# Kernel tuning notes

Hardware: AMD Instinct MI355X
Metric: run time of the kernel (lower is better)

The kernel has to match this reference:

```python
import jax, jax.numpy as jnp
import numpy as np

ITERATION = 10

def setup_inputs() -> dict:
    key = jax.random.key(0)
    k1, k2, k3 = jax.random.split(key, 3)
    a_inter = jax.random.normal(k1, (8, 64, 64, 32, 32), dtype=jnp.float32)
    logits = jax.random.normal(k2, (8, 64), dtype=jnp.float32)
    W = jax.random.normal(k3, (1, 64, 64), dtype=jnp.float32)
    return {"a_inter": a_inter, "logits": logits, "W": W}


def reference(a_inter, logits, W):
    N = W.shape[1]  # num_nodes
    B = a_inter.shape[0]
    # feats: [B, N, C*H*W]
    feats = a_inter[:, :, :N, :, :].reshape(B, N, -1)
    # expand logits [B, N] -> [B, N, N] (unsqueeze(1).expand in torch)
    logits0 = jnp.broadcast_to(logits[:, None, :], (B, N, N))

    feats_norm = jnp.linalg.norm(feats, ord=2, axis=2, keepdims=True)  # [B, N, 1]
    pairwise_norm = feats_norm @ jnp.swapaxes(feats_norm, 1, 2)        # [B, N, N]
    pairwise_dot = feats @ jnp.swapaxes(feats, 1, 2)                   # [B, N, N]
    pairwise_sim = pairwise_dot / (pairwise_norm + 1e-6)
    W_sym = (W + jnp.swapaxes(W, 1, 2)) / 2.0
    pairwise_potential = pairwise_sim * W_sym                          # [B, N, N]

    unary_potential = logits0

    def body(i, l):
        probs = jnp.swapaxes(jax.nn.sigmoid(l), 1, 2)  # [B, N, N]
        # probs*pp - (1-probs)*pp == (2*probs - 1)*pp
        pp_E = jnp.sum((2.0 * probs - 1.0) * pairwise_potential, axis=2, keepdims=True)
        return unary_potential + pp_E

    logits_out = jax.lax.fori_loop(0, ITERATION, body, logits0)
    return logits_out.mean(axis=1)  # [B, N]
```

## Files before the change

### kernel.cpp

```cpp
#include <hip/hip_runtime.h>
#include <math.h>

#define BATCH 8
#define NN 64
#define DD 65536
#define BPB 64
#define NBLK (BATCH * BPB)
#define KC (DD / BPB)
#define KW (KC / 4)
#define KSTEPS (KW / 32)
#define NTRI 10
#define PSZ (NTRI * 256)

typedef float  floatx4 __attribute__((ext_vector_type(4)));
typedef __bf16 bf16x8  __attribute__((ext_vector_type(8)));

static __device__ __forceinline__ bf16x8 cvt8(float4 lo, float4 hi) {
    const unsigned sel = 0x07060302u;
    union { unsigned u[4]; bf16x8 v; } r;
    r.u[0] = __builtin_amdgcn_perm(__float_as_uint(lo.y), __float_as_uint(lo.x), sel);
    r.u[1] = __builtin_amdgcn_perm(__float_as_uint(lo.w), __float_as_uint(lo.z), sel);
    r.u[2] = __builtin_amdgcn_perm(__float_as_uint(hi.y), __float_as_uint(hi.x), sel);
    r.u[3] = __builtin_amdgcn_perm(__float_as_uint(hi.w), __float_as_uint(hi.z), sel);
    return r.v;
}

__global__ __launch_bounds__(256, 2) void gram_partial_kernel(const float* __restrict__ a,
                                                              float* __restrict__ part) {
    __shared__ __align__(16) float red[3][NTRI][64][4];

    const int bid = blockIdx.x;
    const int b = bid >> 6;
    const int c = bid & (BPB - 1);

    const int tid  = threadIdx.x;
    const int w    = tid >> 6;
    const int lane = tid & 63;
    const int m    = lane & 15;
    const int q    = lane >> 4;

    const float* base = a + (size_t)b * NN * DD + (size_t)c * KC + (size_t)w * KW
                          + (size_t)m * DD + q * 8;
    const float* p0 = base;
    const float* p1 = base + (size_t)16 * DD;
    const float* p2 = base + (size_t)32 * DD;
    const float* p3 = base + (size_t)48 * DD;

    floatx4 acc[NTRI];
    #pragma unroll
    for (int i = 0; i < NTRI; ++i) acc[i] = (floatx4)0.0f;

    float4 A0, A1, A2, A3, A4, A5, A6, A7;
    float4 B0, B1, B2, B3, B4, B5, B6, B7;

#define LOADSET(R0,R1,R2,R3,R4,R5,R6,R7, o)                                \
    R0 = *(const float4*)(p0 + (o));  R1 = *(const float4*)(p0 + (o) + 4); \
    R2 = *(const float4*)(p1 + (o));  R3 = *(const float4*)(p1 + (o) + 4); \
    R4 = *(const float4*)(p2 + (o));  R5 = *(const float4*)(p2 + (o) + 4); \
    R6 = *(const float4*)(p3 + (o));  R7 = *(const float4*)(p3 + (o) + 4); \
    __builtin_amdgcn_sched_barrier(0);

#define MFMASET(R0,R1,R2,R3,R4,R5,R6,R7)                                   \
    {                                                                      \
        bf16x8 f0 = cvt8(R0, R1);                                          \
        bf16x8 f1 = cvt8(R2, R3);                                          \
        bf16x8 f2 = cvt8(R4, R5);                                          \
        bf16x8 f3 = cvt8(R6, R7);                                          \
        acc[0] = __builtin_amdgcn_mfma_f32_16x16x32_bf16(f0, f0, acc[0], 0, 0, 0); \
        acc[1] = __builtin_amdgcn_mfma_f32_16x16x32_bf16(f0, f1, acc[1], 0, 0, 0); \
        acc[2] = __builtin_amdgcn_mfma_f32_16x16x32_bf16(f0, f2, acc[2], 0, 0, 0); \
        acc[3] = __builtin_amdgcn_mfma_f32_16x16x32_bf16(f0, f3, acc[3], 0, 0, 0); \
        acc[4] = __builtin_amdgcn_mfma_f32_16x16x32_bf16(f1, f1, acc[4], 0, 0, 0); \
        acc[5] = __builtin_amdgcn_mfma_f32_16x16x32_bf16(f1, f2, acc[5], 0, 0, 0); \
        acc[6] = __builtin_amdgcn_mfma_f32_16x16x32_bf16(f1, f3, acc[6], 0, 0, 0); \
        acc[7] = __builtin_amdgcn_mfma_f32_16x16x32_bf16(f2, f2, acc[7], 0, 0, 0); \
        acc[8] = __builtin_amdgcn_mfma_f32_16x16x32_bf16(f2, f3, acc[8], 0, 0, 0); \
        acc[9] = __builtin_amdgcn_mfma_f32_16x16x32_bf16(f3, f3, acc[9], 0, 0, 0); \
    }

    LOADSET(A0,A1,A2,A3,A4,A5,A6,A7, 0)
    #pragma unroll
    for (int s = 0; s < KSTEPS; s += 2) {
        LOADSET(B0,B1,B2,B3,B4,B5,B6,B7, (s + 1) * 32)
        MFMASET(A0,A1,A2,A3,A4,A5,A6,A7)
        if (s + 2 < KSTEPS) { LOADSET(A0,A1,A2,A3,A4,A5,A6,A7, (s + 2) * 32) }
        MFMASET(B0,B1,B2,B3,B4,B5,B6,B7)
    }
#undef LOADSET
#undef MFMASET

    if (w > 0) {
        #pragma unroll
        for (int t = 0; t < NTRI; ++t)
            *(floatx4*)&red[w - 1][t][lane][0] = acc[t];
    }
    __syncthreads();
    if (w == 0) {
        #pragma unroll
        for (int t = 0; t < NTRI; ++t) {
            floatx4 r0 = *(const floatx4*)&red[0][t][lane][0];
            floatx4 r1 = *(const floatx4*)&red[1][t][lane][0];
            floatx4 r2 = *(const floatx4*)&red[2][t][lane][0];
            acc[t] += (r0 + r1) + r2;
        }
        float* pg = part + (size_t)bid * PSZ;
        #pragma unroll
        for (int t = 0; t < NTRI; ++t) {
            float* tp = pg + t * 256 + m;
            #pragma unroll
            for (int r = 0; r < 4; ++r)
                tp[(q * 4 + r) * 16] = acc[t][r];
        }
    }
}

__global__ __launch_bounds__(128) void gram_reduce_kernel(const float* __restrict__ part,
                                                          float* __restrict__ gram) {
    const int gid = blockIdx.x * 128 + threadIdx.x;
    const int b   = gid >> 12;
    const int idx = gid & 4095;
    const int i   = idx >> 6;
    const int j   = idx & 63;
    const int ti  = i >> 4, tj = j >> 4;
    const int ib  = ti <= tj ? ti : tj;
    const int jb  = ti <= tj ? tj : ti;
    const int slot = ib * 4 - (ib * (ib - 1)) / 2 + (jb - ib);
    const int rr  = (ti <= tj) ? (i & 15) : (j & 15);
    const int cc  = (ti <= tj) ? (j & 15) : (i & 15);
    const int off = slot * 256 + rr * 16 + cc;
    const float* p = part + (size_t)b * BPB * PSZ + off;

    float s0 = 0.f, s1 = 0.f, s2 = 0.f, s3 = 0.f;
    #pragma unroll 4
    for (int c = 0; c < BPB; c += 4) {
        s0 += p[(size_t)(c + 0) * PSZ];
        s1 += p[(size_t)(c + 1) * PSZ];
        s2 += p[(size_t)(c + 2) * PSZ];
        s3 += p[(size_t)(c + 3) * PSZ];
    }
    gram[gid] = (s0 + s1) + (s2 + s3);
}

__global__ __launch_bounds__(256) void crf_kernel(const float* __restrict__ gram,
                                                  const float* __restrict__ logits,
                                                  const float* __restrict__ Wm,
                                                  float* __restrict__ out) {
    __shared__ float pp[NN][NN + 1];
    __shared__ float E[NN];
    __shared__ float nrm[NN];
    __shared__ float part[4 * NN];

    const int b  = blockIdx.x;
    const int tid = threadIdx.x;
    const int i  = tid & 63;
    const int jq = tid >> 6;
    const float* g = gram + b * NN * NN;

    if (jq == 0) nrm[i] = sqrtf(g[i * NN + i]);
    E[i] = 0.0f;
    __syncthreads();

    const float ni = nrm[i];
    for (int jj = 0; jj < 16; ++jj) {
        int j = jq * 16 + jj;
        float wsym = 0.5f * (Wm[i * NN + j] + Wm[j * NN + i]);
        pp[i][j] = g[i * NN + j] / (ni * nrm[j] + 1e-6f) * wsym;
    }
    const float li = logits[b * NN + i];
    __syncthreads();

    for (int it = 0; it < 10; ++it) {
        float acc = 0.0f;
        for (int jj = 0; jj < 16; ++jj) {
            int j = jq * 16 + jj;
            float t = li + E[j];
            float s = 1.0f / (1.0f + expf(-t));
            acc = fmaf(2.0f * s - 1.0f, pp[i][j], acc);
        }
        part[jq * NN + i] = acc;
        __syncthreads();
        if (jq == 0)
            E[i] = part[i] + part[NN + i] + part[2 * NN + i] + part[3 * NN + i];
        __syncthreads();
    }

    if (tid < 64) {
        float s = E[tid];
        for (int off = 32; off > 0; off >>= 1) s += __shfl_down(s, off);
        float meanE = __shfl(s, 0) * (1.0f / 64.0f);
        out[b * NN + tid] = logits[b * NN + tid] + meanE;
    }
}

extern "C" void kernel_launch(void* const* d_in, const int* in_sizes, int n_in,
                              void* d_out, int out_size, void* d_ws, size_t ws_size,
                              hipStream_t stream) {
    const float* a      = (const float*)d_in[0];
    const float* logits = (const float*)d_in[1];
    const float* Wm     = (const float*)d_in[2];
    float* out  = (float*)d_out;

    float* part = (float*)d_ws;
    float* gram = part + (size_t)NBLK * PSZ;

    gram_partial_kernel<<<NBLK, 256, 0, stream>>>(a, part);
    gram_reduce_kernel<<<(BATCH * NN * NN) / 128, 128, 0, stream>>>(part, gram);
    crf_kernel<<<BATCH, 256, 0, stream>>>(gram, logits, Wm, out);
}
```

Measured before the change: 220.3 us.

## Stage bf16-converted tiles through double-buffered LDS with coalesced row loads

Global loads are changed so each half-wavefront reads a contiguous 512-byte row segment, instead of each lane reading scattered 32-byte pieces from four rows. The values are converted to bf16 and written to a swizzled, double-buffered shared-memory tile, and MFMA operands are then read back from LDS. The goal is better global coalescing and less VGPR pressure for in-flight loads. In exchange it adds LDS traffic, a barrier per stage and the LDS footprint of the double buffer.

```diff
diff --git a/kernel.cpp b/kernel.cpp
--- a/kernel.cpp
+++ b/kernel.cpp
@@ -7,27 +7,20 @@
 #define BPB 64
 #define NBLK (BATCH * BPB)
 #define KC (DD / BPB)
-#define KW (KC / 4)
-#define KSTEPS (KW / 32)
+#define BKF 128
+#define NSTG (KC / BKF)
 #define NTRI 10
 #define PSZ (NTRI * 256)
 
 typedef float  floatx4 __attribute__((ext_vector_type(4)));
 typedef __bf16 bf16x8  __attribute__((ext_vector_type(8)));
 
-static __device__ __forceinline__ bf16x8 cvt8(float4 lo, float4 hi) {
-    const unsigned sel = 0x07060302u;
-    union { unsigned u[4]; bf16x8 v; } r;
-    r.u[0] = __builtin_amdgcn_perm(__float_as_uint(lo.y), __float_as_uint(lo.x), sel);
-    r.u[1] = __builtin_amdgcn_perm(__float_as_uint(lo.w), __float_as_uint(lo.z), sel);
-    r.u[2] = __builtin_amdgcn_perm(__float_as_uint(hi.y), __float_as_uint(hi.x), sel);
-    r.u[3] = __builtin_amdgcn_perm(__float_as_uint(hi.w), __float_as_uint(hi.z), sel);
-    return r.v;
-}
-
 __global__ __launch_bounds__(256, 2) void gram_partial_kernel(const float* __restrict__ a,
                                                               float* __restrict__ part) {
-    __shared__ __align__(16) float red[3][NTRI][64][4];
+    __shared__ __align__(16) union {
+        unsigned char buf[2][64 * 256];
+        float red[3][NTRI][64][4];
+    } sh;
 
     const int bid = blockIdx.x;
     const int b = bid >> 6;
@@ -39,33 +32,52 @@
     const int m    = lane & 15;
     const int q    = lane >> 4;
 
-    const float* base = a + (size_t)b * NN * DD + (size_t)c * KC + (size_t)w * KW
-                          + (size_t)m * DD + q * 8;
-    const float* p0 = base;
-    const float* p1 = base + (size_t)16 * DD;
-    const float* p2 = base + (size_t)32 * DD;
-    const float* p3 = base + (size_t)48 * DD;
+    const int h  = tid >> 5;
+    const int cl = tid & 31;
+    const float* gp = a + (size_t)b * NN * DD + (size_t)h * DD
+                        + (size_t)c * KC + cl * 4;
+    const int wb = h * 256 + ((cl * 8) ^ (h << 4));
+
+    const int colr = ((w * 64 + q * 16) ^ ((m & 7) << 4));
+
+    const unsigned sel = 0x07060302u;
 
     floatx4 acc[NTRI];
     #pragma unroll
     for (int i = 0; i < NTRI; ++i) acc[i] = (floatx4)0.0f;
 
-    float4 A0, A1, A2, A3, A4, A5, A6, A7;
-    float4 B0, B1, B2, B3, B4, B5, B6, B7;
-
-#define LOADSET(R0,R1,R2,R3,R4,R5,R6,R7, o)                                \
-    R0 = *(const float4*)(p0 + (o));  R1 = *(const float4*)(p0 + (o) + 4); \
-    R2 = *(const float4*)(p1 + (o));  R3 = *(const float4*)(p1 + (o) + 4); \
-    R4 = *(const float4*)(p2 + (o));  R5 = *(const float4*)(p2 + (o) + 4); \
-    R6 = *(const float4*)(p3 + (o));  R7 = *(const float4*)(p3 + (o) + 4); \
-    __builtin_amdgcn_sched_barrier(0);
-
-#define MFMASET(R0,R1,R2,R3,R4,R5,R6,R7)                                   \
-    {                                                                      \
-        bf16x8 f0 = cvt8(R0, R1);                                          \
-        bf16x8 f1 = cvt8(R2, R3);                                          \
-        bf16x8 f2 = cvt8(R4, R5);                                          \
-        bf16x8 f3 = cvt8(R6, R7);                                          \
+    float4 L0, L1, L2, L3, L4, L5, L6, L7;
+
+#define LOADS(s)                                                            \
+    L0 = *(const float4*)(gp + (size_t)0 * 8 * DD + (s) * BKF);             \
+    L1 = *(const float4*)(gp + (size_t)1 * 8 * DD + (s) * BKF);             \
+    L2 = *(const float4*)(gp + (size_t)2 * 8 * DD + (s) * BKF);             \
+    L3 = *(const float4*)(gp + (size_t)3 * 8 * DD + (s) * BKF);             \
+    L4 = *(const float4*)(gp + (size_t)4 * 8 * DD + (s) * BKF);             \
+    L5 = *(const float4*)(gp + (size_t)5 * 8 * DD + (s) * BKF);             \
+    L6 = *(const float4*)(gp + (size_t)6 * 8 * DD + (s) * BKF);             \
+    L7 = *(const float4*)(gp + (size_t)7 * 8 * DD + (s) * BKF);
+
+#define PUT1(bs, j, Lj)                                                     \
+    {                                                                       \
+        unsigned lo_ = __builtin_amdgcn_perm(__float_as_uint(Lj.y),         \
+                                             __float_as_uint(Lj.x), sel);   \
+        unsigned hi_ = __builtin_amdgcn_perm(__float_as_uint(Lj.w),         \
+                                             __float_as_uint(Lj.z), sel);   \
+        *(uint2*)&sh.buf[bs][(j) * 2048 + wb] = make_uint2(lo_, hi_);       \
+    }
+
+#define PUTALL(bs)                                                          \
+    PUT1(bs, 0, L0) PUT1(bs, 1, L1) PUT1(bs, 2, L2) PUT1(bs, 3, L3)         \
+    PUT1(bs, 4, L4) PUT1(bs, 5, L5) PUT1(bs, 6, L6) PUT1(bs, 7, L7)
+
+#define COMPUTE(bs)                                                         \
+    {                                                                       \
+        const unsigned char* tb = sh.buf[bs];                               \
+        bf16x8 f0 = *(const bf16x8*)(tb + (m     ) * 256 + colr);           \
+        bf16x8 f1 = *(const bf16x8*)(tb + (m + 16) * 256 + colr);           \
+        bf16x8 f2 = *(const bf16x8*)(tb + (m + 32) * 256 + colr);           \
+        bf16x8 f3 = *(const bf16x8*)(tb + (m + 48) * 256 + colr);           \
         acc[0] = __builtin_amdgcn_mfma_f32_16x16x32_bf16(f0, f0, acc[0], 0, 0, 0); \
         acc[1] = __builtin_amdgcn_mfma_f32_16x16x32_bf16(f0, f1, acc[1], 0, 0, 0); \
         acc[2] = __builtin_amdgcn_mfma_f32_16x16x32_bf16(f0, f2, acc[2], 0, 0, 0); \
@@ -78,29 +90,35 @@
         acc[9] = __builtin_amdgcn_mfma_f32_16x16x32_bf16(f3, f3, acc[9], 0, 0, 0); \
     }
 
-    LOADSET(A0,A1,A2,A3,A4,A5,A6,A7, 0)
+    LOADS(0)
+    PUTALL(0)
+    __syncthreads();
+
     #pragma unroll
-    for (int s = 0; s < KSTEPS; s += 2) {
-        LOADSET(B0,B1,B2,B3,B4,B5,B6,B7, (s + 1) * 32)
-        MFMASET(A0,A1,A2,A3,A4,A5,A6,A7)
-        if (s + 2 < KSTEPS) { LOADSET(A0,A1,A2,A3,A4,A5,A6,A7, (s + 2) * 32) }
-        MFMASET(B0,B1,B2,B3,B4,B5,B6,B7)
-    }
-#undef LOADSET
-#undef MFMASET
+    for (int s = 0; s < NSTG; ++s) {
+        if (s + 1 < NSTG) { LOADS(s + 1) }
+        __builtin_amdgcn_sched_barrier(0);
+        COMPUTE(s & 1)
+        if (s + 1 < NSTG) { PUTALL((s + 1) & 1) }
+        __syncthreads();
+    }
+#undef LOADS
+#undef PUT1
+#undef PUTALL
+#undef COMPUTE
 
     if (w > 0) {
         #pragma unroll
         for (int t = 0; t < NTRI; ++t)
-            *(floatx4*)&red[w - 1][t][lane][0] = acc[t];
+            *(floatx4*)&sh.red[w - 1][t][lane][0] = acc[t];
     }
     __syncthreads();
     if (w == 0) {
         #pragma unroll
         for (int t = 0; t < NTRI; ++t) {
-            floatx4 r0 = *(const floatx4*)&red[0][t][lane][0];
-            floatx4 r1 = *(const floatx4*)&red[1][t][lane][0];
-            floatx4 r2 = *(const floatx4*)&red[2][t][lane][0];
+            floatx4 r0 = *(const floatx4*)&sh.red[0][t][lane][0];
+            floatx4 r1 = *(const floatx4*)&sh.red[1][t][lane][0];
+            floatx4 r2 = *(const floatx4*)&sh.red[2][t][lane][0];
             acc[t] += (r0 + r1) + r2;
         }
         float* pg = part + (size_t)bid * PSZ;
```

Measured after the change: 223.1 us. Within noise of the previous version (+1.3%).
